# Performance work log

Hardware: AMD Instinct MI355X
Metric: run time of the kernel (lower is better)

The kernel has to match this reference:

```python
import jax, jax.numpy as jnp
import numpy as np
from jax import lax

H = 64  # hidden size of both LSTM layers


def _lstm(x, W_ih, W_hh, b_ih, b_hh):
    """Single-layer batch-first LSTM (torch gate order i,f,g,o).
    x: [B,S,F]; returns (all_h [B,S,H], last_h [B,H])."""
    B, S, _ = x.shape
    # Precompute input projections for all timesteps at once: [B,S,4H]
    xp = jnp.einsum('bsf,gf->bsg', x, W_ih) + b_ih + b_hh

    def step(carry, xt):  # xt: [B,4H]
        h, c = carry
        z = xt + h @ W_hh.T
        i, f, g, o = jnp.split(z, 4, axis=-1)
        i = jax.nn.sigmoid(i)
        f = jax.nn.sigmoid(f)
        g = jnp.tanh(g)
        o = jax.nn.sigmoid(o)
        c = f * c + i * g
        h = o * jnp.tanh(c)
        return (h, c), h

    h0 = jnp.zeros((B, H), x.dtype)
    c0 = jnp.zeros((B, H), x.dtype)
    (h_last, _), hs = lax.scan(step, (h0, c0), jnp.swapaxes(xp, 0, 1))
    return jnp.swapaxes(hs, 0, 1), h_last


def setup_inputs() -> dict:
    key = jax.random.key(0)
    ks = jax.random.split(key, 14)
    B, S, F, OUT = 4096, 512, 1, 24
    s = 1.0 / np.sqrt(H)  # torch default uniform bound ~ 1/sqrt(hidden)
    r = lambda k, shape: jax.random.uniform(k, shape, jnp.float32, -s, s)
    return {
        'x': jax.random.normal(ks[0], (B, S, F), jnp.float32),
        'W_ih1': r(ks[1], (4 * H, F)),
        'W_hh1': r(ks[2], (4 * H, H)),
        'b_ih1': r(ks[3], (4 * H,)),
        'b_hh1': r(ks[4], (4 * H,)),
        'W_ih2': r(ks[5], (4 * H, H)),
        'W_hh2': r(ks[6], (4 * H, H)),
        'b_ih2': r(ks[7], (4 * H,)),
        'b_hh2': r(ks[8], (4 * H,)),
        'W_d1': r(ks[9], (32, H)),
        'b_d1': r(ks[10], (32,)),
        'W_d2': r(ks[11], (OUT, 32)),
        'b_d2': r(ks[12], (OUT,)),
    }


def reference(x, W_ih1, W_hh1, b_ih1, b_hh1, W_ih2, W_hh2, b_ih2, b_hh2,
              W_d1, b_d1, W_d2, b_d2):
    h1, _ = _lstm(x, W_ih1, W_hh1, b_ih1, b_hh1)          # [B,S,64]
    # dropout1 is identity in eval mode
    _, h_last = _lstm(h1, W_ih2, W_hh2, b_ih2, b_hh2)     # [B,64]
    # dropout2 is identity in eval mode
    y = jax.nn.relu(h_last @ W_d1.T + b_d1)                # [B,32]
    return y @ W_d2.T + b_d2                               # [B,24]
```

## Files before the change

### kernel.cpp

```cpp
#include <hip/hip_runtime.h>


typedef __attribute__((ext_vector_type(8))) short bf16x8;
typedef __attribute__((ext_vector_type(4))) float floatx4;

#define SEQ 512
#define HID 64
#define LOG2E 1.4426950408889634f

__device__ inline floatx4 MFMA(bf16x8 a, bf16x8 b, floatx4 c) {
    return __builtin_amdgcn_mfma_f32_16x16x32_bf16(a, b, c, 0, 0, 0);
}
__device__ inline short f2bf(float f) {
    __bf16 b = (__bf16)f;
    return __builtin_bit_cast(short, b);
}
__device__ inline float exp2_fast(float x) {
#if __has_builtin(__builtin_amdgcn_exp2f)
    return __builtin_amdgcn_exp2f(x);
#else
    return __expf(x * 0.6931471805599453f);
#endif
}
__device__ inline float rcp_fast(float x) { return __builtin_amdgcn_rcpf(x); }

__device__ inline float lstm_gate(float zi, float zf, float zg, float zo, float& c) {
    float ei = exp2_fast(zi);
    float ef = exp2_fast(zf);
    float eg = exp2_fast(zg);
    float eo = exp2_fast(zo);
    float sf = rcp_fast(1.0f + ef);
    float ig = (1.0f - eg) * rcp_fast((1.0f + ei) * (1.0f + eg));
    c = sf * c + ig;
    float ec = exp2_fast(fminf(c * (-2.0f * LOG2E), 40.0f));
    return (1.0f - ec) * rcp_fast((1.0f + eo) * (1.0f + ec));
}

__global__ __launch_bounds__(256, 1) void lstm_fused(
    const float* __restrict__ x,
    const float* __restrict__ Wih1, const float* __restrict__ Whh1,
    const float* __restrict__ bih1, const float* __restrict__ bhh1,
    const float* __restrict__ Wih2, const float* __restrict__ Whh2,
    const float* __restrict__ bih2, const float* __restrict__ bhh2,
    const float* __restrict__ Wd1,  const float* __restrict__ bd1,
    const float* __restrict__ Wd2,  const float* __restrict__ bd2,
    float* __restrict__ out)
{
    const int tid  = threadIdx.x;
    const int wave = tid >> 6;
    const int lane = tid & 63;
    const int l15  = lane & 15;
    const int quad = lane >> 4;
    const int b0   = blockIdx.x * 16;

    __shared__ __align__(16) float x_s[16][516];
    __shared__ __align__(16) short h1_s[2][16][72];
    __shared__ __align__(16) short h2_s[2][16][72];
    __shared__ float y1_s[16][32];

    {
        const int row = tid >> 4;
        const int c0  = (tid & 15) * 32;
        const float4* src = reinterpret_cast<const float4*>(x + (size_t)(b0 + row) * SEQ + c0);
        float4* dst = reinterpret_cast<float4*>(&x_s[row][c0]);
        #pragma unroll
        for (int j = 0; j < 8; ++j) dst[j] = src[j];
    }
    for (int i = tid; i < 2 * 16 * 72; i += 256) {
        (&h1_s[0][0][0])[i] = 0;
        (&h2_s[0][0][0])[i] = 0;
    }

    bf16x8 Bhh1[2][4], Bih2[2][4], Bhh2[2][4];
    float wih1c[4], b1c[4], b2c[4];
    #pragma unroll
    for (int g = 0; g < 4; ++g) {
        const float sc = (g == 2) ? (-2.0f * LOG2E) : (-LOG2E);
        const int col = g * 64 + wave * 16 + l15;
        wih1c[g] = Wih1[col] * sc;
        b1c[g]   = (bih1[col] + bhh1[col]) * sc;
        b2c[g]   = (bih2[col] + bhh2[col]) * sc;
        #pragma unroll
        for (int kt = 0; kt < 2; ++kt) {
            const int koff = kt * 32 + quad * 8;
            union { short s[8]; bf16x8 v; } u1, u2, u3;
            #pragma unroll
            for (int j = 0; j < 8; ++j) {
                u1.s[j] = f2bf(Whh1[col * HID + koff + j] * sc);
                u2.s[j] = f2bf(Wih2[col * HID + koff + j] * sc);
                u3.s[j] = f2bf(Whh2[col * HID + koff + j] * sc);
            }
            Bhh1[kt][g] = u1.v; Bih2[kt][g] = u2.v; Bhh2[kt][g] = u3.v;
        }
    }

    const int hcol = wave * 16 + l15;
    float c1[4] = {0, 0, 0, 0}, c2[4] = {0, 0, 0, 0};

    #pragma unroll 2
    for (int t = 0; t < SEQ; ++t) {
        const int pr1 = (t + 1) & 1;
        const int pr2 = t & 1;
        __syncthreads();
        const bf16x8 A1a = *reinterpret_cast<const bf16x8*>(&h1_s[pr1][l15][quad * 8]);
        const bf16x8 A1b = *reinterpret_cast<const bf16x8*>(&h1_s[pr1][l15][32 + quad * 8]);
        const bf16x8 A2a = *reinterpret_cast<const bf16x8*>(&h2_s[pr2][l15][quad * 8]);
        const bf16x8 A2b = *reinterpret_cast<const bf16x8*>(&h2_s[pr2][l15][32 + quad * 8]);

        floatx4 z1[4], z2[4];
        #pragma unroll
        for (int g = 0; g < 4; ++g) {
            #pragma unroll
            for (int r = 0; r < 4; ++r)
                z1[g][r] = x_s[quad * 4 + r][t] * wih1c[g] + b1c[g];
            z2[g] = floatx4{b2c[g], b2c[g], b2c[g], b2c[g]};
        }
        #pragma unroll
        for (int g = 0; g < 4; ++g) {
            z1[g] = MFMA(A1a, Bhh1[0][g], z1[g]);
            z1[g] = MFMA(A1b, Bhh1[1][g], z1[g]);
            z2[g] = MFMA(A1a, Bih2[0][g], z2[g]);
            z2[g] = MFMA(A1b, Bih2[1][g], z2[g]);
            z2[g] = MFMA(A2a, Bhh2[0][g], z2[g]);
            z2[g] = MFMA(A2b, Bhh2[1][g], z2[g]);
        }

        const float m2 = (t == 0) ? 0.0f : 1.0f;
        #pragma unroll
        for (int r = 0; r < 4; ++r) {
            float h1v = lstm_gate(z1[0][r], z1[1][r], z1[2][r], z1[3][r], c1[r]);
            h1_s[pr2][quad * 4 + r][hcol] = f2bf(h1v);
            float cc = c2[r];
            float h2v = lstm_gate(z2[0][r], z2[1][r], z2[2][r], z2[3][r], cc) * m2;
            c2[r] = cc * m2;
            h2_s[pr1][quad * 4 + r][hcol] = f2bf(h2v);
        }
    }

    __syncthreads();
    {
        const bf16x8 A1a = *reinterpret_cast<const bf16x8*>(&h1_s[1][l15][quad * 8]);
        const bf16x8 A1b = *reinterpret_cast<const bf16x8*>(&h1_s[1][l15][32 + quad * 8]);
        const bf16x8 A2a = *reinterpret_cast<const bf16x8*>(&h2_s[0][l15][quad * 8]);
        const bf16x8 A2b = *reinterpret_cast<const bf16x8*>(&h2_s[0][l15][32 + quad * 8]);
        floatx4 z2[4];
        #pragma unroll
        for (int g = 0; g < 4; ++g) {
            z2[g] = floatx4{b2c[g], b2c[g], b2c[g], b2c[g]};
            z2[g] = MFMA(A1a, Bih2[0][g], z2[g]);
            z2[g] = MFMA(A1b, Bih2[1][g], z2[g]);
            z2[g] = MFMA(A2a, Bhh2[0][g], z2[g]);
            z2[g] = MFMA(A2b, Bhh2[1][g], z2[g]);
        }
        float* h2f = &x_s[0][0];
        #pragma unroll
        for (int r = 0; r < 4; ++r) {
            float cc = c2[r];
            float h2v = lstm_gate(z2[0][r], z2[1][r], z2[2][r], z2[3][r], cc);
            h2f[(quad * 4 + r) * HID + hcol] = h2v;
        }
    }
    __syncthreads();

    const float* h2f = &x_s[0][0];
    for (int idx = tid; idx < 16 * 32; idx += 256) {
        const int b = idx >> 5, o = idx & 31;
        float acc = bd1[o];
        #pragma unroll 8
        for (int k = 0; k < HID; ++k) acc += h2f[b * HID + k] * Wd1[o * HID + k];
        y1_s[b][o] = fmaxf(acc, 0.0f);
    }
    __syncthreads();
    for (int idx = tid; idx < 16 * 24; idx += 256) {
        const int b = idx / 24, o = idx - b * 24;
        float acc = bd2[o];
        #pragma unroll 8
        for (int k = 0; k < 32; ++k) acc += y1_s[b][k] * Wd2[o * 32 + k];
        out[(size_t)(b0 + b) * 24 + o] = acc;
    }
}

extern "C" void kernel_launch(void* const* d_in, const int* in_sizes, int n_in,
                              void* d_out, int out_size, void* d_ws, size_t ws_size,
                              hipStream_t stream) {
    const float* x    = (const float*)d_in[0];
    const float* Wih1 = (const float*)d_in[1];
    const float* Whh1 = (const float*)d_in[2];
    const float* bih1 = (const float*)d_in[3];
    const float* bhh1 = (const float*)d_in[4];
    const float* Wih2 = (const float*)d_in[5];
    const float* Whh2 = (const float*)d_in[6];
    const float* bih2 = (const float*)d_in[7];
    const float* bhh2 = (const float*)d_in[8];
    const float* Wd1  = (const float*)d_in[9];
    const float* bd1  = (const float*)d_in[10];
    const float* Wd2  = (const float*)d_in[11];
    const float* bd2  = (const float*)d_in[12];
    float* out = (float*)d_out;

    lstm_fused<<<256, 256, 0, stream>>>(x, Wih1, Whh1, bih1, bhh1,
                                        Wih2, Whh2, bih2, bhh2,
                                        Wd1, bd1, Wd2, bd2, out);
}
```

Before: 507.5 us.

## Split LSTM layers across dedicated wave groups with 512-thread blocks

Doubles the block to 8 waves. Waves 0-3 compute layer 1 and waves 4-7 compute layer 2, instead of every wave computing both layers serially. Each wave now holds only its own weight fragments and one cell state, which cuts per-wave MFMA and gate work per timestep. The gate update is also rewritten so the sigmoid(f) and input-gate reciprocals are merged into a single reciprocal. The cost is that layer-1 waves issue only half the MFMAs of layer-2 waves, so that group idles at each barrier, and block-wide syncs now span 8 waves.

After: 465.5 us. -8.3%, faster.

```diff
diff --git a/kernel.cpp b/kernel.cpp
--- a/kernel.cpp
+++ b/kernel.cpp
@@ -29,14 +29,15 @@
     float ef = exp2_fast(zf);
     float eg = exp2_fast(zg);
     float eo = exp2_fast(zo);
-    float sf = rcp_fast(1.0f + ef);
-    float ig = (1.0f - eg) * rcp_fast((1.0f + ei) * (1.0f + eg));
-    c = sf * c + ig;
+    float P  = (1.0f + ei) * (1.0f + eg);
+    float F  = 1.0f + ef;
+    float num = c * P + (1.0f - eg) * F;
+    c = num * rcp_fast(P * F);
     float ec = exp2_fast(fminf(c * (-2.0f * LOG2E), 40.0f));
     return (1.0f - ec) * rcp_fast((1.0f + eo) * (1.0f + ec));
 }
 
-__global__ __launch_bounds__(256, 1) void lstm_fused(
+__global__ __launch_bounds__(512, 2) void lstm_fused(
     const float* __restrict__ x,
     const float* __restrict__ Wih1, const float* __restrict__ Whh1,
     const float* __restrict__ bih1, const float* __restrict__ bhh1,
@@ -48,6 +49,8 @@
 {
     const int tid  = threadIdx.x;
     const int wave = tid >> 6;
+    const int ct   = wave & 3;
+    const int is2  = wave >> 2;
     const int lane = tid & 63;
     const int l15  = lane & 15;
     const int quad = lane >> 4;
@@ -59,111 +62,131 @@
     __shared__ float y1_s[16][32];
 
     {
-        const int row = tid >> 4;
-        const int c0  = (tid & 15) * 32;
+        const int row = tid >> 5;
+        const int c0  = (tid & 31) * 16;
         const float4* src = reinterpret_cast<const float4*>(x + (size_t)(b0 + row) * SEQ + c0);
         float4* dst = reinterpret_cast<float4*>(&x_s[row][c0]);
         #pragma unroll
-        for (int j = 0; j < 8; ++j) dst[j] = src[j];
-    }
-    for (int i = tid; i < 2 * 16 * 72; i += 256) {
+        for (int j = 0; j < 4; ++j) dst[j] = src[j];
+    }
+    for (int i = tid; i < 2 * 16 * 72; i += 512) {
         (&h1_s[0][0][0])[i] = 0;
         (&h2_s[0][0][0])[i] = 0;
     }
 
-    bf16x8 Bhh1[2][4], Bih2[2][4], Bhh2[2][4];
-    float wih1c[4], b1c[4], b2c[4];
+    bf16x8 Wf[4][4];
+    float wxc[4], bcs[4];
     #pragma unroll
     for (int g = 0; g < 4; ++g) {
         const float sc = (g == 2) ? (-2.0f * LOG2E) : (-LOG2E);
-        const int col = g * 64 + wave * 16 + l15;
-        wih1c[g] = Wih1[col] * sc;
-        b1c[g]   = (bih1[col] + bhh1[col]) * sc;
-        b2c[g]   = (bih2[col] + bhh2[col]) * sc;
+        const int col = g * 64 + ct * 16 + l15;
+        if (!is2) {
+            wxc[g] = Wih1[col] * sc;
+            bcs[g] = (bih1[col] + bhh1[col]) * sc;
+        } else {
+            wxc[g] = 0.0f;
+            bcs[g] = (bih2[col] + bhh2[col]) * sc;
+        }
         #pragma unroll
         for (int kt = 0; kt < 2; ++kt) {
             const int koff = kt * 32 + quad * 8;
-            union { short s[8]; bf16x8 v; } u1, u2, u3;
+            union { short s[8]; bf16x8 v; } u0, u1;
             #pragma unroll
             for (int j = 0; j < 8; ++j) {
-                u1.s[j] = f2bf(Whh1[col * HID + koff + j] * sc);
-                u2.s[j] = f2bf(Wih2[col * HID + koff + j] * sc);
-                u3.s[j] = f2bf(Whh2[col * HID + koff + j] * sc);
-            }
-            Bhh1[kt][g] = u1.v; Bih2[kt][g] = u2.v; Bhh2[kt][g] = u3.v;
-        }
-    }
-
-    const int hcol = wave * 16 + l15;
-    float c1[4] = {0, 0, 0, 0}, c2[4] = {0, 0, 0, 0};
+                if (!is2) {
+                    u0.s[j] = f2bf(Whh1[col * HID + koff + j] * sc);
+                    u1.s[j] = 0;
+                } else {
+                    u0.s[j] = f2bf(Wih2[col * HID + koff + j] * sc);
+                    u1.s[j] = f2bf(Whh2[col * HID + koff + j] * sc);
+                }
+            }
+            Wf[kt][g] = u0.v;
+            Wf[2 + kt][g] = u1.v;
+        }
+    }
+
+    const int hcol = ct * 16 + l15;
+    float cst[4] = {0, 0, 0, 0};
 
     #pragma unroll 2
     for (int t = 0; t < SEQ; ++t) {
         const int pr1 = (t + 1) & 1;
         const int pr2 = t & 1;
         __syncthreads();
-        const bf16x8 A1a = *reinterpret_cast<const bf16x8*>(&h1_s[pr1][l15][quad * 8]);
-        const bf16x8 A1b = *reinterpret_cast<const bf16x8*>(&h1_s[pr1][l15][32 + quad * 8]);
-        const bf16x8 A2a = *reinterpret_cast<const bf16x8*>(&h2_s[pr2][l15][quad * 8]);
-        const bf16x8 A2b = *reinterpret_cast<const bf16x8*>(&h2_s[pr2][l15][32 + quad * 8]);
-
-        floatx4 z1[4], z2[4];
-        #pragma unroll
-        for (int g = 0; g < 4; ++g) {
-            #pragma unroll
-            for (int r = 0; r < 4; ++r)
-                z1[g][r] = x_s[quad * 4 + r][t] * wih1c[g] + b1c[g];
-            z2[g] = floatx4{b2c[g], b2c[g], b2c[g], b2c[g]};
-        }
-        #pragma unroll
-        for (int g = 0; g < 4; ++g) {
-            z1[g] = MFMA(A1a, Bhh1[0][g], z1[g]);
-            z1[g] = MFMA(A1b, Bhh1[1][g], z1[g]);
-            z2[g] = MFMA(A1a, Bih2[0][g], z2[g]);
-            z2[g] = MFMA(A1b, Bih2[1][g], z2[g]);
-            z2[g] = MFMA(A2a, Bhh2[0][g], z2[g]);
-            z2[g] = MFMA(A2b, Bhh2[1][g], z2[g]);
-        }
-
-        const float m2 = (t == 0) ? 0.0f : 1.0f;
-        #pragma unroll
-        for (int r = 0; r < 4; ++r) {
-            float h1v = lstm_gate(z1[0][r], z1[1][r], z1[2][r], z1[3][r], c1[r]);
-            h1_s[pr2][quad * 4 + r][hcol] = f2bf(h1v);
-            float cc = c2[r];
-            float h2v = lstm_gate(z2[0][r], z2[1][r], z2[2][r], z2[3][r], cc) * m2;
-            c2[r] = cc * m2;
-            h2_s[pr1][quad * 4 + r][hcol] = f2bf(h2v);
+        if (!is2) {
+            const bf16x8 A1a = *reinterpret_cast<const bf16x8*>(&h1_s[pr1][l15][quad * 8]);
+            const bf16x8 A1b = *reinterpret_cast<const bf16x8*>(&h1_s[pr1][l15][32 + quad * 8]);
+            floatx4 z[4];
+            #pragma unroll
+            for (int g = 0; g < 4; ++g)
+                #pragma unroll
+                for (int r = 0; r < 4; ++r)
+                    z[g][r] = x_s[quad * 4 + r][t] * wxc[g] + bcs[g];
+            #pragma unroll
+            for (int g = 0; g < 4; ++g) {
+                z[g] = MFMA(A1a, Wf[0][g], z[g]);
+                z[g] = MFMA(A1b, Wf[1][g], z[g]);
+            }
+            #pragma unroll
+            for (int r = 0; r < 4; ++r) {
+                float h1v = lstm_gate(z[0][r], z[1][r], z[2][r], z[3][r], cst[r]);
+                h1_s[pr2][quad * 4 + r][hcol] = f2bf(h1v);
+            }
+        } else {
+            const bf16x8 A1a = *reinterpret_cast<const bf16x8*>(&h1_s[pr1][l15][quad * 8]);
+            const bf16x8 A1b = *reinterpret_cast<const bf16x8*>(&h1_s[pr1][l15][32 + quad * 8]);
+            const bf16x8 A2a = *reinterpret_cast<const bf16x8*>(&h2_s[pr2][l15][quad * 8]);
+            const bf16x8 A2b = *reinterpret_cast<const bf16x8*>(&h2_s[pr2][l15][32 + quad * 8]);
+            floatx4 z[4];
+            #pragma unroll
+            for (int g = 0; g < 4; ++g)
+                z[g] = floatx4{bcs[g], bcs[g], bcs[g], bcs[g]};
+            #pragma unroll
+            for (int g = 0; g < 4; ++g) {
+                z[g] = MFMA(A1a, Wf[0][g], z[g]);
+                z[g] = MFMA(A1b, Wf[1][g], z[g]);
+                z[g] = MFMA(A2a, Wf[2][g], z[g]);
+                z[g] = MFMA(A2b, Wf[3][g], z[g]);
+            }
+            const float m2 = (t == 0) ? 0.0f : 1.0f;
+            #pragma unroll
+            for (int r = 0; r < 4; ++r) {
+                float cc = cst[r];
+                float h2v = lstm_gate(z[0][r], z[1][r], z[2][r], z[3][r], cc) * m2;
+                cst[r] = cc * m2;
+                h2_s[pr1][quad * 4 + r][hcol] = f2bf(h2v);
+            }
         }
     }
 
     __syncthreads();
-    {
+    if (is2) {
         const bf16x8 A1a = *reinterpret_cast<const bf16x8*>(&h1_s[1][l15][quad * 8]);
         const bf16x8 A1b = *reinterpret_cast<const bf16x8*>(&h1_s[1][l15][32 + quad * 8]);
         const bf16x8 A2a = *reinterpret_cast<const bf16x8*>(&h2_s[0][l15][quad * 8]);
         const bf16x8 A2b = *reinterpret_cast<const bf16x8*>(&h2_s[0][l15][32 + quad * 8]);
-        floatx4 z2[4];
+        floatx4 z[4];
         #pragma unroll
         for (int g = 0; g < 4; ++g) {
-            z2[g] = floatx4{b2c[g], b2c[g], b2c[g], b2c[g]};
-            z2[g] = MFMA(A1a, Bih2[0][g], z2[g]);
-            z2[g] = MFMA(A1b, Bih2[1][g], z2[g]);
-            z2[g] = MFMA(A2a, Bhh2[0][g], z2[g]);
-            z2[g] = MFMA(A2b, Bhh2[1][g], z2[g]);
+            z[g] = floatx4{bcs[g], bcs[g], bcs[g], bcs[g]};
+            z[g] = MFMA(A1a, Wf[0][g], z[g]);
+            z[g] = MFMA(A1b, Wf[1][g], z[g]);
+            z[g] = MFMA(A2a, Wf[2][g], z[g]);
+            z[g] = MFMA(A2b, Wf[3][g], z[g]);
         }
         float* h2f = &x_s[0][0];
         #pragma unroll
         for (int r = 0; r < 4; ++r) {
-            float cc = c2[r];
-            float h2v = lstm_gate(z2[0][r], z2[1][r], z2[2][r], z2[3][r], cc);
+            float cc = cst[r];
+            float h2v = lstm_gate(z[0][r], z[1][r], z[2][r], z[3][r], cc);
             h2f[(quad * 4 + r) * HID + hcol] = h2v;
         }
     }
     __syncthreads();
 
     const float* h2f = &x_s[0][0];
-    for (int idx = tid; idx < 16 * 32; idx += 256) {
+    for (int idx = tid; idx < 16 * 32; idx += 512) {
         const int b = idx >> 5, o = idx & 31;
         float acc = bd1[o];
         #pragma unroll 8
@@ -171,7 +194,7 @@
         y1_s[b][o] = fmaxf(acc, 0.0f);
     }
     __syncthreads();
-    for (int idx = tid; idx < 16 * 24; idx += 256) {
+    for (int idx = tid; idx < 16 * 24; idx += 512) {
         const int b = idx / 24, o = idx - b * 24;
         float acc = bd2[o];
         #pragma unroll 8
@@ -198,7 +221,7 @@
     const float* bd2  = (const float*)d_in[12];
     float* out = (float*)d_out;
 
-    lstm_fused<<<256, 256, 0, stream>>>(x, Wih1, Whh1, bih1, bhh1,
+    lstm_fused<<<256, 512, 0, stream>>>(x, Wih1, Whh1, bih1, bhh1,
                                         Wih2, Whh2, bih2, bhh2,
                                         Wd1, bd1, Wd2, bd2, out);
 }
```
